# Performance work log

Hardware: AMD Instinct MI355X
Metric: run time of the kernel (lower is better)

Reference implementation:

```python
import jax, jax.numpy as jnp
import numpy as np

B, IH, IW, C = 128, 16, 16, 1024   # weighted_context NHWC; idf = IH*IW = 256
S, EMB, IDF = 32, 256, 256


def setup_inputs() -> dict:
    key = jax.random.key(0)
    k1, k2, k3 = jax.random.split(key, 3)
    return {
        "weighted_context": jax.random.normal(k1, (B, IH, IW, C), dtype=jnp.float32),
        "word_emb": jax.random.normal(k2, (B, S, EMB), dtype=jnp.float32),
        "conv_kernel": jax.random.normal(k3, (EMB, IDF), dtype=jnp.float32) * (1.0 / np.sqrt(EMB)),
        "conv_bias": jnp.zeros((IDF,), dtype=jnp.float32),
    }


def reference(weighted_context, word_emb, conv_kernel, conv_bias):
    b, ih, iw, c = weighted_context.shape
    s = word_emb.shape[1]
    # 1x1 conv over the (expanded) word embeddings == per-token linear projection
    we = jnp.einsum("bse,ei->bsi", word_emb, conv_kernel) + conv_bias  # [B, S, idf]
    wc = weighted_context.reshape(b, ih * iw, c)                        # [B, HW, C]
    # matmul(wc, we, transpose_a=True, transpose_b=True): contracts HW with idf (idf == HW)
    attn = jnp.einsum("bpc,bsp->bcs", wc, we)                           # [B, C, S]
    # reshape to [B*C, S] + softmax == softmax over last axis
    attn = jax.nn.softmax(attn, axis=-1)
    # matmul(we^T [B, idf, S], attn^T [B, S, C]) -> [B, idf, C]
    out = jnp.einsum("bsp,bcs->bpc", we, attn).reshape(b, ih, iw, c)
    return (out, attn)
```

## Files before the change

### kernel.cpp

```cpp
#include <hip/hip_runtime.h>


typedef float  f32x4  __attribute__((ext_vector_type(4)));
typedef short  bf16x8 __attribute__((ext_vector_type(8)));

namespace {
constexpr int kB = 128, kHW = 256, kC = 1024, kS = 32, kE = 256;
constexpr int WR = 40;
}

__device__ inline ushort f2bf(float x) {
  unsigned u = __float_as_uint(x);
  u += 0x7fffu + ((u >> 16) & 1u);
  return (ushort)(u >> 16);
}
__device__ inline float bf2f(ushort h) { return __uint_as_float(((unsigned)h) << 16); }

#define MFMA16(A, Bf, Cv) __builtin_amdgcn_mfma_f32_16x16x32_bf16((A), (Bf), (Cv), 0, 0, 0)

__global__ __launch_bounds__(256) void we_proj_kernel(
    const float* __restrict__ emb, const float* __restrict__ K,
    const float* __restrict__ bias, ushort* __restrict__ wTh,
    ushort* __restrict__ wTl) {
  const int b  = blockIdx.y;
  const int sq = blockIdx.x;
  const int p  = threadIdx.x;

  __shared__ float embS[kE][8];
  {
    const float* src = emb + (size_t)b * kS * kE + (size_t)sq * 8 * kE;
    const int j  = threadIdx.x >> 5;
    const int e4 = (threadIdx.x & 31) * 8;
#pragma unroll
    for (int u = 0; u < 8; ++u) embS[e4 + u][j] = src[j * kE + e4 + u];
  }
  __syncthreads();

  float acc[8];
#pragma unroll
  for (int j = 0; j < 8; ++j) acc[j] = 0.f;

#pragma unroll 4
  for (int e = 0; e < kE; ++e) {
    const float kv = K[e * kHW + p];
    const float4 e0 = *(const float4*)&embS[e][0];
    const float4 e1 = *(const float4*)&embS[e][4];
    acc[0] = fmaf(e0.x, kv, acc[0]); acc[1] = fmaf(e0.y, kv, acc[1]);
    acc[2] = fmaf(e0.z, kv, acc[2]); acc[3] = fmaf(e0.w, kv, acc[3]);
    acc[4] = fmaf(e1.x, kv, acc[4]); acc[5] = fmaf(e1.y, kv, acc[5]);
    acc[6] = fmaf(e1.z, kv, acc[6]); acc[7] = fmaf(e1.w, kv, acc[7]);
  }

  const float bv = bias[p];
  bf16x8 hv, lv;
#pragma unroll
  for (int j = 0; j < 8; ++j) {
    const float x = acc[j] + bv;
    const ushort h = f2bf(x);
    hv[j] = (short)h;
    lv[j] = (short)f2bf(x - bf2f(h));
  }
  const size_t o = ((size_t)b * kHW + p) * kS + sq * 8;
  *(bf16x8*)(wTh + o) = hv;
  *(bf16x8*)(wTl + o) = lv;
}

__global__ __launch_bounds__(256, 2) void attn_kernel(
    const float* __restrict__ wc, const ushort* __restrict__ wTh,
    const ushort* __restrict__ wTl, float* __restrict__ out,
    float* __restrict__ attn_out) {
  const int b    = blockIdx.y;
  const int cb   = blockIdx.x * 256;
  const int tid  = threadIdx.x;
  const int wave = tid >> 6, lane = tid & 63;
  const int lr   = lane & 15, lg = lane >> 4;

  __shared__ ushort wH[kHW][WR], wL[kHW][WR];
  __shared__ ushort pH[256][WR], pL[256][WR];

  {
    const bf16x8* sh = (const bf16x8*)(wTh + ((size_t)b * kHW + tid) * kS);
    const bf16x8* sl = (const bf16x8*)(wTl + ((size_t)b * kHW + tid) * kS);
#pragma unroll
    for (int k = 0; k < 4; ++k) {
      *(bf16x8*)&wH[tid][k * 8] = sh[k];
      *(bf16x8*)&wL[tid][k * 8] = sl[k];
    }
  }
  __syncthreads();

  const float* wcb = wc + (size_t)b * kHW * kC;
  const int c0 = cb + wave * 64;

  f32x4 acc[4][2];
#pragma unroll
  for (int m = 0; m < 4; ++m)
#pragma unroll
    for (int n = 0; n < 2; ++n) acc[m][n] = (f32x4){0.f, 0.f, 0.f, 0.f};

  float avC[8], avN[8];
#pragma unroll
  for (int i = 0; i < 8; ++i)
    avC[i] = wcb[(size_t)(lg * 8 + i) * kC + c0 + lr];

#pragma unroll 1
  for (int kt = 0; kt < 8; ++kt) {
    bf16x8 bh[2], bl[2];
#pragma unroll
    for (int n = 0; n < 2; ++n)
#pragma unroll
      for (int j = 0; j < 8; ++j) {
        const int row = kt * 32 + lg * 8 + j;
        bh[n][j] = (short)wH[row][n * 16 + lr];
        bl[n][j] = (short)wL[row][n * 16 + lr];
      }
#pragma unroll
    for (int m = 0; m < 4; ++m) {
      const int mn  = (m + 1) & 3;
      const int ktn = (m == 3) ? kt + 1 : kt;
      if (!(kt == 7 && m == 3)) {
#pragma unroll
        for (int i = 0; i < 8; ++i)
          avN[i] = wcb[(size_t)(ktn * 32 + lg * 8 + i) * kC + c0 + mn * 16 + lr];
      }
      bf16x8 ah, al;
#pragma unroll
      for (int i = 0; i < 8; ++i) {
        const ushort h = f2bf(avC[i]);
        ah[i] = (short)h;
        al[i] = (short)f2bf(avC[i] - bf2f(h));
      }
#pragma unroll
      for (int n = 0; n < 2; ++n) {
        acc[m][n] = MFMA16(ah, bh[n], acc[m][n]);
        acc[m][n] = MFMA16(ah, bl[n], acc[m][n]);
        acc[m][n] = MFMA16(al, bh[n], acc[m][n]);
      }
#pragma unroll
      for (int i = 0; i < 8; ++i) avC[i] = avN[i];
    }
  }

  float* attnb = attn_out + ((size_t)b * kC + cb) * kS;
#pragma unroll
  for (int m = 0; m < 4; ++m) {
#pragma unroll
    for (int j = 0; j < 4; ++j) {
      float v0 = acc[m][0][j], v1 = acc[m][1][j];
      float mx = fmaxf(v0, v1);
      mx = fmaxf(mx, __shfl_xor(mx, 1));
      mx = fmaxf(mx, __shfl_xor(mx, 2));
      mx = fmaxf(mx, __shfl_xor(mx, 4));
      mx = fmaxf(mx, __shfl_xor(mx, 8));
      float e0 = __expf(v0 - mx), e1 = __expf(v1 - mx);
      float sm = e0 + e1;
      sm += __shfl_xor(sm, 1); sm += __shfl_xor(sm, 2);
      sm += __shfl_xor(sm, 4); sm += __shfl_xor(sm, 8);
      const float inv = 1.f / sm;
      e0 *= inv; e1 *= inv;
      const int cL = wave * 64 + m * 16 + lg * 4 + j;
      attnb[(size_t)cL * kS + lr]      = e0;
      attnb[(size_t)cL * kS + 16 + lr] = e1;
      const ushort h0 = f2bf(e0);
      pH[cL][lr] = h0;           pL[cL][lr] = f2bf(e0 - bf2f(h0));
      const ushort h1 = f2bf(e1);
      pH[cL][16 + lr] = h1;      pL[cL][16 + lr] = f2bf(e1 - bf2f(h1));
    }
  }

  bf16x8 pbh[4], pbl[4];
#pragma unroll
  for (int n = 0; n < 4; ++n) {
    const int cL = wave * 64 + n * 16 + lr;
    pbh[n] = *(const bf16x8*)&pH[cL][lg * 8];
    pbl[n] = *(const bf16x8*)&pL[cL][lg * 8];
  }
  float* outb = out + (size_t)b * kHW * kC + cb;
#pragma unroll 1
  for (int pt = 0; pt < 16; ++pt) {
    const int pr = pt * 16 + lr;
    const bf16x8 ah = *(const bf16x8*)&wH[pr][lg * 8];
    const bf16x8 al = *(const bf16x8*)&wL[pr][lg * 8];
#pragma unroll
    for (int n = 0; n < 4; ++n) {
      f32x4 o = (f32x4){0.f, 0.f, 0.f, 0.f};
      o = MFMA16(ah, pbh[n], o);
      o = MFMA16(ah, pbl[n], o);
      o = MFMA16(al, pbh[n], o);
      const int ccol = wave * 64 + n * 16 + lr;
#pragma unroll
      for (int j = 0; j < 4; ++j)
        outb[(size_t)(pt * 16 + lg * 4 + j) * kC + ccol] = o[j];
    }
  }
}

extern "C" void kernel_launch(void* const* d_in, const int* in_sizes, int n_in,
                              void* d_out, int out_size, void* d_ws, size_t ws_size,
                              hipStream_t stream) {
  const float* wc   = (const float*)d_in[0];
  const float* emb  = (const float*)d_in[1];
  const float* K    = (const float*)d_in[2];
  const float* bias = (const float*)d_in[3];

  float* out  = (float*)d_out;
  float* attn = out + (size_t)kB * kHW * kC;
  ushort* wTh = (ushort*)d_ws;
  ushort* wTl = wTh + (size_t)kB * kHW * kS;

  we_proj_kernel<<<dim3(4, kB), 256, 0, stream>>>(emb, K, bias, wTh, wTl);
  attn_kernel<<<dim3(4, kB), 256, 0, stream>>>(wc, wTh, wTl, out, attn);
}
```

Before: 83.13 us.

## Fuse word-embedding projection into attention kernel and use single-bf16 output matmul

Drops the separate projection kernel and its workspace round trip. Each block now recomputes the 32x256 projected embedding with split-bf16 MFMA directly into LDS. The result is stored transposed, so B-fragment loads become vector reads instead of scalar gathers. The second matmul (we^T · softmax) now uses only the high bf16 parts, cutting its MFMA count by a factor of three at some cost in precision. The projection is redundantly recomputed by the 4 blocks per batch, and its K-matrix reads are strided scalar global loads.

```diff
diff --git a/kernel.cpp b/kernel.cpp
--- a/kernel.cpp
+++ b/kernel.cpp
@@ -6,7 +6,8 @@
 
 namespace {
 constexpr int kB = 128, kHW = 256, kC = 1024, kS = 32, kE = 256;
-constexpr int WR = 40;
+constexpr int TP = kHW + 8;
+constexpr int WR = kS + 8;
 }
 
 __device__ inline ushort f2bf(float x) {
@@ -18,102 +19,106 @@
 
 #define MFMA16(A, Bf, Cv) __builtin_amdgcn_mfma_f32_16x16x32_bf16((A), (Bf), (Cv), 0, 0, 0)
 
-__global__ __launch_bounds__(256) void we_proj_kernel(
-    const float* __restrict__ emb, const float* __restrict__ K,
-    const float* __restrict__ bias, ushort* __restrict__ wTh,
-    ushort* __restrict__ wTl) {
-  const int b  = blockIdx.y;
-  const int sq = blockIdx.x;
-  const int p  = threadIdx.x;
-
-  __shared__ float embS[kE][8];
-  {
-    const float* src = emb + (size_t)b * kS * kE + (size_t)sq * 8 * kE;
-    const int j  = threadIdx.x >> 5;
-    const int e4 = (threadIdx.x & 31) * 8;
-#pragma unroll
-    for (int u = 0; u < 8; ++u) embS[e4 + u][j] = src[j * kE + e4 + u];
-  }
-  __syncthreads();
-
-  float acc[8];
-#pragma unroll
-  for (int j = 0; j < 8; ++j) acc[j] = 0.f;
-
-#pragma unroll 4
-  for (int e = 0; e < kE; ++e) {
-    const float kv = K[e * kHW + p];
-    const float4 e0 = *(const float4*)&embS[e][0];
-    const float4 e1 = *(const float4*)&embS[e][4];
-    acc[0] = fmaf(e0.x, kv, acc[0]); acc[1] = fmaf(e0.y, kv, acc[1]);
-    acc[2] = fmaf(e0.z, kv, acc[2]); acc[3] = fmaf(e0.w, kv, acc[3]);
-    acc[4] = fmaf(e1.x, kv, acc[4]); acc[5] = fmaf(e1.y, kv, acc[5]);
-    acc[6] = fmaf(e1.z, kv, acc[6]); acc[7] = fmaf(e1.w, kv, acc[7]);
-  }
-
-  const float bv = bias[p];
-  bf16x8 hv, lv;
-#pragma unroll
-  for (int j = 0; j < 8; ++j) {
-    const float x = acc[j] + bv;
-    const ushort h = f2bf(x);
-    hv[j] = (short)h;
-    lv[j] = (short)f2bf(x - bf2f(h));
-  }
-  const size_t o = ((size_t)b * kHW + p) * kS + sq * 8;
-  *(bf16x8*)(wTh + o) = hv;
-  *(bf16x8*)(wTl + o) = lv;
-}
-
-__global__ __launch_bounds__(256, 2) void attn_kernel(
-    const float* __restrict__ wc, const ushort* __restrict__ wTh,
-    const ushort* __restrict__ wTl, float* __restrict__ out,
-    float* __restrict__ attn_out) {
+__global__ __launch_bounds__(256, 2) void fused_attn_kernel(
+    const float* __restrict__ wc, const float* __restrict__ emb,
+    const float* __restrict__ Km, const float* __restrict__ bias,
+    float* __restrict__ out, float* __restrict__ attn_out) {
   const int b    = blockIdx.y;
   const int cb   = blockIdx.x * 256;
   const int tid  = threadIdx.x;
   const int wave = tid >> 6, lane = tid & 63;
   const int lr   = lane & 15, lg = lane >> 4;
 
-  __shared__ ushort wH[kHW][WR], wL[kHW][WR];
-  __shared__ ushort pH[256][WR], pL[256][WR];
-
-  {
-    const bf16x8* sh = (const bf16x8*)(wTh + ((size_t)b * kHW + tid) * kS);
-    const bf16x8* sl = (const bf16x8*)(wTl + ((size_t)b * kHW + tid) * kS);
-#pragma unroll
-    for (int k = 0; k < 4; ++k) {
-      *(bf16x8*)&wH[tid][k * 8] = sh[k];
-      *(bf16x8*)&wL[tid][k * 8] = sl[k];
-    }
-  }
-  __syncthreads();
+  __shared__ ushort wHT[kS][TP];
+  __shared__ ushort wLT[kS][TP];
+  __shared__ ushort wHp[kHW][WR];
+  __shared__ ushort pHl[kHW][WR];
 
   const float* wcb = wc + (size_t)b * kHW * kC;
   const int c0 = cb + wave * 64;
 
-  f32x4 acc[4][2];
-#pragma unroll
-  for (int m = 0; m < 4; ++m)
-#pragma unroll
-    for (int n = 0; n < 2; ++n) acc[m][n] = (f32x4){0.f, 0.f, 0.f, 0.f};
-
   float avC[8], avN[8];
 #pragma unroll
   for (int i = 0; i < 8; ++i)
     avC[i] = wcb[(size_t)(lg * 8 + i) * kC + c0 + lr];
+
+  {
+    const float* embb = emb + (size_t)b * kS * kE;
+    f32x4 pcc[2][4];
+#pragma unroll
+    for (int m = 0; m < 2; ++m)
+#pragma unroll
+      for (int n = 0; n < 4; ++n) pcc[m][n] = (f32x4){0.f, 0.f, 0.f, 0.f};
+
+#pragma unroll 1
+    for (int kt = 0; kt < 8; ++kt) {
+      bf16x8 eah[2], eal[2];
+#pragma unroll
+      for (int m = 0; m < 2; ++m) {
+        const float* ep = embb + (size_t)(m * 16 + lr) * kE + kt * 32 + lg * 8;
+        const float4 v0 = *(const float4*)ep;
+        const float4 v1 = *(const float4*)(ep + 4);
+        const float ev[8] = {v0.x, v0.y, v0.z, v0.w, v1.x, v1.y, v1.z, v1.w};
+#pragma unroll
+        for (int i = 0; i < 8; ++i) {
+          const ushort h = f2bf(ev[i]);
+          eah[m][i] = (short)h;
+          eal[m][i] = (short)f2bf(ev[i] - bf2f(h));
+        }
+      }
+#pragma unroll
+      for (int n = 0; n < 4; ++n) {
+        const int pg = wave * 64 + n * 16 + lr;
+        bf16x8 kh, kl;
+#pragma unroll
+        for (int i = 0; i < 8; ++i) {
+          const float kv = Km[(size_t)(kt * 32 + lg * 8 + i) * kHW + pg];
+          const ushort h = f2bf(kv);
+          kh[i] = (short)h;
+          kl[i] = (short)f2bf(kv - bf2f(h));
+        }
+#pragma unroll
+        for (int m = 0; m < 2; ++m) {
+          pcc[m][n] = MFMA16(eah[m], kh, pcc[m][n]);
+          pcc[m][n] = MFMA16(eah[m], kl, pcc[m][n]);
+          pcc[m][n] = MFMA16(eal[m], kh, pcc[m][n]);
+        }
+      }
+    }
+#pragma unroll
+    for (int n = 0; n < 4; ++n) {
+      const int pg = wave * 64 + n * 16 + lr;
+      const float bv = bias[pg];
+#pragma unroll
+      for (int m = 0; m < 2; ++m)
+#pragma unroll
+        for (int j = 0; j < 4; ++j) {
+          const float x = pcc[m][n][j] + bv;
+          const ushort h = f2bf(x);
+          const ushort l = f2bf(x - bf2f(h));
+          const int s = m * 16 + lg * 4 + j;
+          wHT[s][pg] = h;
+          wLT[s][pg] = l;
+          wHp[pg][s] = h;
+        }
+    }
+  }
+  __syncthreads();
+
+  f32x4 acc[4][2];
+#pragma unroll
+  for (int m = 0; m < 4; ++m)
+#pragma unroll
+    for (int n = 0; n < 2; ++n) acc[m][n] = (f32x4){0.f, 0.f, 0.f, 0.f};
 
 #pragma unroll 1
   for (int kt = 0; kt < 8; ++kt) {
     bf16x8 bh[2], bl[2];
 #pragma unroll
-    for (int n = 0; n < 2; ++n)
-#pragma unroll
-      for (int j = 0; j < 8; ++j) {
-        const int row = kt * 32 + lg * 8 + j;
-        bh[n][j] = (short)wH[row][n * 16 + lr];
-        bl[n][j] = (short)wL[row][n * 16 + lr];
-      }
+    for (int n = 0; n < 2; ++n) {
+      bh[n] = *(const bf16x8*)&wHT[n * 16 + lr][kt * 32 + lg * 8];
+      bl[n] = *(const bf16x8*)&wLT[n * 16 + lr][kt * 32 + lg * 8];
+    }
 #pragma unroll
     for (int m = 0; m < 4; ++m) {
       const int mn  = (m + 1) & 3;
@@ -161,32 +166,24 @@
       const int cL = wave * 64 + m * 16 + lg * 4 + j;
       attnb[(size_t)cL * kS + lr]      = e0;
       attnb[(size_t)cL * kS + 16 + lr] = e1;
-      const ushort h0 = f2bf(e0);
-      pH[cL][lr] = h0;           pL[cL][lr] = f2bf(e0 - bf2f(h0));
-      const ushort h1 = f2bf(e1);
-      pH[cL][16 + lr] = h1;      pL[cL][16 + lr] = f2bf(e1 - bf2f(h1));
-    }
-  }
-
-  bf16x8 pbh[4], pbl[4];
-#pragma unroll
-  for (int n = 0; n < 4; ++n) {
-    const int cL = wave * 64 + n * 16 + lr;
-    pbh[n] = *(const bf16x8*)&pH[cL][lg * 8];
-    pbl[n] = *(const bf16x8*)&pL[cL][lg * 8];
-  }
+      pHl[cL][lr]      = f2bf(e0);
+      pHl[cL][16 + lr] = f2bf(e1);
+    }
+  }
+
+  bf16x8 pbh[4];
+#pragma unroll
+  for (int n = 0; n < 4; ++n)
+    pbh[n] = *(const bf16x8*)&pHl[wave * 64 + n * 16 + lr][lg * 8];
+
   float* outb = out + (size_t)b * kHW * kC + cb;
 #pragma unroll 1
   for (int pt = 0; pt < 16; ++pt) {
-    const int pr = pt * 16 + lr;
-    const bf16x8 ah = *(const bf16x8*)&wH[pr][lg * 8];
-    const bf16x8 al = *(const bf16x8*)&wL[pr][lg * 8];
+    const bf16x8 ah = *(const bf16x8*)&wHp[pt * 16 + lr][lg * 8];
 #pragma unroll
     for (int n = 0; n < 4; ++n) {
       f32x4 o = (f32x4){0.f, 0.f, 0.f, 0.f};
       o = MFMA16(ah, pbh[n], o);
-      o = MFMA16(ah, pbl[n], o);
-      o = MFMA16(al, pbh[n], o);
       const int ccol = wave * 64 + n * 16 + lr;
 #pragma unroll
       for (int j = 0; j < 4; ++j)
@@ -200,14 +197,11 @@
                               hipStream_t stream) {
   const float* wc   = (const float*)d_in[0];
   const float* emb  = (const float*)d_in[1];
-  const float* K    = (const float*)d_in[2];
+  const float* Km   = (const float*)d_in[2];
   const float* bias = (const float*)d_in[3];
 
   float* out  = (float*)d_out;
   float* attn = out + (size_t)kB * kHW * kC;
-  ushort* wTh = (ushort*)d_ws;
-  ushort* wTl = wTh + (size_t)kB * kHW * kS;
-
-  we_proj_kernel<<<dim3(4, kB), 256, 0, stream>>>(emb, K, bias, wTh, wTl);
-  attn_kernel<<<dim3(4, kB), 256, 0, stream>>>(wc, wTh, wTl, out, attn);
-}
+
+  fused_attn_kernel<<<dim3(4, kB), 256, 0, stream>>>(wc, emb, Km, bias, out, attn);
+}
```

Result: no change. 83.21 us (+0.1%).
